# Optimization experiments

Measured on AMD Instinct MI355X. Metric: run time of the kernel, lower is better.

## Reference

```python
import jax, jax.numpy as jnp
import numpy as np

N, P, C, H, W = 2, 100, 256, 128, 192
K = 3; KK = K * K; E = C * KK; NH = 8; DH = E // NH; FFN = 2048


def _ln(x, g, b, eps=1e-5):
    m = x.mean(-1, keepdims=True)
    v = ((x - m) ** 2).mean(-1, keepdims=True)
    return (x - m) * jax.lax.rsqrt(v + eps) * g + b


def setup_inputs():
    ks = iter(jax.random.split(jax.random.key(0), 64))
    def rnd(shape, s=1.0):
        return jax.random.normal(next(ks), shape, jnp.float32) * s
    z = lambda *s: jnp.zeros(s, jnp.float32)
    o = lambda *s: jnp.ones(s, jnp.float32)
    return {
        'x': rnd((N, C, H, W)),
        'proposal_feat': rnd((N, P, E)),
        'mask_preds': rnd((N, P, H, W)),
        'ku_dyn_w': rnd((2 * C, C), 0.02), 'ku_dyn_b': z(2 * C),
        'ku_in_w': rnd((2 * C, C), 0.02), 'ku_in_b': z(2 * C),
        'ku_ig_w': rnd((C, C), 0.02), 'ku_ig_b': z(C),
        'ku_ug_w': rnd((C, C), 0.02), 'ku_ug_b': z(C),
        'ku_nin_g': o(C), 'ku_nin_b': z(C),
        'ku_nout_g': o(C), 'ku_nout_b': z(C),
        'ku_inin_g': o(C), 'ku_inin_b': z(C),
        'ku_inout_g': o(C), 'ku_inout_b': z(C),
        'ku_fc_w': rnd((C, C), 0.02), 'ku_fc_b': z(C),
        'ku_fcn_g': o(C), 'ku_fcn_b': z(C),
        'attn_in_w': rnd((3 * E, E), 0.02), 'attn_in_b': z(3 * E),
        'attn_out_w': rnd((E, E), 0.02), 'attn_out_b': z(E),
        'attn_ln_g': o(E), 'attn_ln_b': z(E),
        'ffn_w1': rnd((FFN, C), 0.02), 'ffn_b1': z(FFN),
        'ffn_w2': rnd((C, FFN), 0.02), 'ffn_b2': z(C),
        'ffn_ln_g': o(C), 'ffn_ln_b': z(C),
        'mask_fc_ws': rnd((3, C, C), 0.02),
        'mask_fc_ln_g': o(3, C), 'mask_fc_ln_b': z(3, C),
        'fc_mask_w': rnd((C, C), 0.02), 'fc_mask_b': z(C),
    }


def _forward(x, proposal_feat, mask_preds, ku_dyn_w, ku_dyn_b, ku_in_w, ku_in_b,
             ku_ig_w, ku_ig_b, ku_ug_w, ku_ug_b, ku_nin_g, ku_nin_b, ku_nout_g,
             ku_nout_b, ku_inin_g, ku_inin_b, ku_inout_g, ku_inout_b, ku_fc_w,
             ku_fc_b, ku_fcn_g, ku_fcn_b, attn_in_w, attn_in_b, attn_out_w,
             attn_out_b, attn_ln_g, attn_ln_b, ffn_w1, ffn_b1, ffn_w2, ffn_b2,
             ffn_ln_g, ffn_ln_b, mask_fc_ws, mask_fc_ln_g, mask_fc_ln_b,
             fc_mask_w, fc_mask_b):
    # mask-softmax pooling over proposals: (N,P,H,W) x (N,C,H,W) -> (N,P,C)
    sig = jax.nn.softmax(mask_preds, axis=1)
    x_feat = jnp.einsum('bnhw,bchw->bnc', sig, x)

    # KernelUpdator (gated dynamic kernel update)
    pf = proposal_feat.reshape(N, P, C, KK).transpose(0, 1, 3, 2).reshape(N * P, KK, C)
    upd = x_feat.reshape(N * P, C)
    params = upd @ ku_dyn_w.T + ku_dyn_b            # (NP, 2C)
    p_in, p_out = params[:, :C], params[:, C:]
    inp = pf @ ku_in_w.T + ku_in_b                  # (NP, KK, 2C)
    i_in, i_out = inp[..., :C], inp[..., C:]
    gate = i_in * p_in[:, None, :]                  # (NP, KK, C)
    ig = jax.nn.sigmoid(_ln(gate @ ku_ig_w.T + ku_ig_b, ku_inin_g, ku_inin_b))
    ug = jax.nn.sigmoid(_ln(gate @ ku_ug_w.T + ku_ug_b, ku_nin_g, ku_nin_b))
    p_out = _ln(p_out, ku_nout_g, ku_nout_b)
    i_out = _ln(i_out, ku_inout_g, ku_inout_b)
    feat = ug * p_out[:, None, :] + ig * i_out
    feat = jax.nn.relu(_ln(feat @ ku_fc_w.T + ku_fc_b, ku_fcn_g, ku_fcn_b))  # (NP,KK,C)

    # self-attention across proposals; embed dim E = C*K*K, with residual + LN
    obj = feat.reshape(N, P, E).transpose(1, 0, 2)  # (P,N,E)
    qkv = obj @ attn_in_w.T + attn_in_b
    q, k, v = jnp.split(qkv, 3, axis=-1)
    q = q.reshape(P, N, NH, DH) * np.float32(1.0 / np.sqrt(DH))
    k = k.reshape(P, N, NH, DH)
    v = v.reshape(P, N, NH, DH)
    a = jax.nn.softmax(jnp.einsum('qnhd,knhd->nhqk', q, k), axis=-1)
    o = jnp.einsum('nhqk,knhd->qnhd', a, v).reshape(P, N, E)
    obj = _ln(obj + o @ attn_out_w.T + attn_out_b, attn_ln_g, attn_ln_b)
    obj = obj.transpose(1, 0, 2).reshape(N, P, KK, C)

    # FFN (residual) + LN, applied per (proposal, kernel position)
    h = jax.nn.relu(obj @ ffn_w1.T + ffn_b1) @ ffn_w2.T + ffn_b2
    obj = _ln(obj + h, ffn_ln_g, ffn_ln_b)

    mf = obj
    for i in range(3):
        mf = jax.nn.relu(_ln(mf @ mask_fc_ws[i].T, mask_fc_ln_g[i], mask_fc_ln_b[i]))
    mf = mf @ fc_mask_w.T + fc_mask_b               # (N,P,KK,C)
    kernels = mf.transpose(0, 1, 3, 2).reshape(N, P, C, K, K)

    # per-image dynamic conv: vmap replaces the python loop over batch
    def conv_one(xi, wi):
        return jax.lax.conv_general_dilated(
            xi[None], wi, (1, 1), 'SAME',
            dimension_numbers=('NCHW', 'OIHW', 'NCHW'))[0]
    new_masks = jax.vmap(conv_one)(x, kernels)      # (N,P,H,W)

    obj_kernels = obj.transpose(0, 1, 3, 2).reshape(N, P, C, K, K)
    return new_masks, obj_kernels


def reference(x, proposal_feat, mask_preds, ku_dyn_w, ku_dyn_b, ku_in_w, ku_in_b,
              ku_ig_w, ku_ig_b, ku_ug_w, ku_ug_b, ku_nin_g, ku_nin_b, ku_nout_g,
              ku_nout_b, ku_inin_g, ku_inin_b, ku_inout_g, ku_inout_b, ku_fc_w,
              ku_fc_b, ku_fcn_g, ku_fcn_b, attn_in_w, attn_in_b, attn_out_w,
              attn_out_b, attn_ln_g, attn_ln_b, ffn_w1, ffn_b1, ffn_w2, ffn_b2,
              ffn_ln_g, ffn_ln_b, mask_fc_ws, mask_fc_ln_g, mask_fc_ln_b,
              fc_mask_w, fc_mask_b):
    return _forward(x, proposal_feat, mask_preds, ku_dyn_w, ku_dyn_b, ku_in_w,
                    ku_in_b, ku_ig_w, ku_ig_b, ku_ug_w, ku_ug_b, ku_nin_g,
                    ku_nin_b, ku_nout_g, ku_nout_b, ku_inin_g, ku_inin_b,
                    ku_inout_g, ku_inout_b, ku_fc_w, ku_fc_b, ku_fcn_g, ku_fcn_b,
                    attn_in_w, attn_in_b, attn_out_w, attn_out_b, attn_ln_g,
                    attn_ln_b, ffn_w1, ffn_b1, ffn_w2, ffn_b2, ffn_ln_g,
                    ffn_ln_b, mask_fc_ws, mask_fc_ln_g, mask_fc_ln_b,
                    fc_mask_w, fc_mask_b)
```

## Files before the change

kernel.cpp:

```cpp
#include <hip/hip_runtime.h>
#include <hip/hip_bf16.h>

#define N_ 2
#define P_ 100
#define C_ 256
#define H_ 128
#define W_ 192
#define HW_ 24576
#define KK_ 9
#define E_ 2304
#define NH_ 8
#define DH_ 288
#define FFN_ 2048
#define NP_ 200
#define ROWS_ 1800
#define XKC_ 64

typedef __attribute__((ext_vector_type(8))) __bf16 bf16x8;
typedef __attribute__((ext_vector_type(4))) float f32x4;

__global__ __launch_bounds__(256) void k_softmax(const float* __restrict__ mp, float* __restrict__ sig){
  int idx = blockIdx.x*256 + threadIdx.x;
  if(idx >= N_*HW_) return;
  int n = idx / HW_, hw = idx - n*HW_;
  const float* base = mp + (size_t)n*P_*HW_ + hw;
  float m = -1e30f;
  for(int p=0;p<P_;p++) m = fmaxf(m, base[(size_t)p*HW_]);
  float s = 0.f;
  for(int p=0;p<P_;p++) s += __expf(base[(size_t)p*HW_] - m);
  float inv = 1.f/s;
  float* ob = sig + (size_t)n*P_*HW_ + hw;
  for(int p=0;p<P_;p++) ob[(size_t)p*HW_] = __expf(base[(size_t)p*HW_] - m)*inv;
}

__global__ __launch_bounds__(256) void k_permute_pf(const float* __restrict__ prop, float* __restrict__ pf){
  int i = blockIdx.x*256 + threadIdx.x;
  if(i >= ROWS_*C_) return;
  int c = i & 255;
  int r = i >> 8;
  int kk = r % 9, np = r / 9;
  pf[i] = prop[(size_t)np*E_ + c*KK_ + kk];
}

__global__ __launch_bounds__(256) void k_xfeat1m(const float* __restrict__ sig, const float* __restrict__ x,
                                                 float* __restrict__ partial){
  const int ct = blockIdx.x, kb = blockIdx.y, n = blockIdx.z;
  const int hw0 = kb*384;
  const int tid = threadIdx.x;
  const int wid = tid >> 6, lane = tid & 63;
  const int col = lane & 15, quad = lane >> 4;
  const int wm = wid & 1, wn = wid >> 1;
  const int MT = wm ? 3 : 4;
  __shared__ __bf16 As[112][72];
  __shared__ __bf16 Bs[128][72];
  f32x4 acc[4][4] = {};
  for(int k0=0; k0<384; k0+=64){
    __syncthreads();
    for(int i=tid; i<896; i+=256){
      int p = i >> 3, kg = i & 7;
      bf16x8 v;
      if(p < P_){
        const float* sp = &sig[((size_t)n*P_ + p)*HW_ + hw0 + k0 + kg*8];
        const float4 f0 = *(const float4*)sp;
        const float4 f1 = *(const float4*)(sp+4);
        v[0]=(__bf16)f0.x; v[1]=(__bf16)f0.y; v[2]=(__bf16)f0.z; v[3]=(__bf16)f0.w;
        v[4]=(__bf16)f1.x; v[5]=(__bf16)f1.y; v[6]=(__bf16)f1.z; v[7]=(__bf16)f1.w;
      } else {
        #pragma unroll
        for(int u=0;u<8;u++) v[u] = (__bf16)0.f;
      }
      *(bf16x8*)&As[p][kg*8] = v;
    }
    for(int i=tid; i<1024; i+=256){
      int c = i >> 3, kg = i & 7;
      const float* xp = &x[((size_t)n*C_ + ct*128 + c)*HW_ + hw0 + k0 + kg*8];
      const float4 f0 = *(const float4*)xp;
      const float4 f1 = *(const float4*)(xp+4);
      bf16x8 v;
      v[0]=(__bf16)f0.x; v[1]=(__bf16)f0.y; v[2]=(__bf16)f0.z; v[3]=(__bf16)f0.w;
      v[4]=(__bf16)f1.x; v[5]=(__bf16)f1.y; v[6]=(__bf16)f1.z; v[7]=(__bf16)f1.w;
      *(bf16x8*)&Bs[c][kg*8] = v;
    }
    __syncthreads();
    #pragma unroll
    for(int ks=0; ks<2; ks++){
      bf16x8 b[4];
      #pragma unroll
      for(int t=0;t<4;t++) b[t] = *(const bf16x8*)&Bs[(wn*4+t)*16 + col][ks*32 + quad*8];
      #pragma unroll
      for(int mt=0; mt<4; mt++){
        if(mt < MT){
          bf16x8 a = *(const bf16x8*)&As[(wm*4+mt)*16 + col][ks*32 + quad*8];
          #pragma unroll
          for(int t=0;t<4;t++)
            acc[mt][t] = __builtin_amdgcn_mfma_f32_16x16x32_bf16(a, b[t], acc[mt][t], 0, 0, 0);
        }
      }
    }
  }
  #pragma unroll
  for(int mt=0; mt<4; mt++){
    if(mt < MT){
      #pragma unroll
      for(int r=0;r<4;r++){
        int p = (wm*4+mt)*16 + quad*4 + r;
        if(p < P_){
          float* op = &partial[(((size_t)n*XKC_ + kb)*P_ + p)*C_ + ct*128 + wn*64 + col];
          #pragma unroll
          for(int t=0;t<4;t++) op[t*16] = acc[mt][t][r];
        }
      }
    }
  }
}

__global__ __launch_bounds__(256) void k_xfeat2(const float* __restrict__ partial, float* __restrict__ xfeat){
  int np = blockIdx.x;
  int n = np / P_, p = np - n*P_;
  int c = threadIdx.x;
  float s = 0.f;
  for(int kb=0;kb<XKC_;kb++) s += partial[(((size_t)n*XKC_ + kb)*P_ + p)*C_ + c];
  xfeat[(size_t)np*C_ + c] = s;
}

__global__ __launch_bounds__(256) void k_gemm_mfma(const float* __restrict__ A, const float* __restrict__ Wt,
    const float* __restrict__ bias, float* __restrict__ out, int M, int N, int K, int act)
{
  const int n0 = blockIdx.x*128, m0 = blockIdx.y*64;
  const int tid = threadIdx.x;
  const int wid = tid >> 6, lane = tid & 63;
  const int col = lane & 15, quad = lane >> 4;
  const int wm = wid & 1, wn = wid >> 1;
  __shared__ __bf16 As[64][72];
  __shared__ __bf16 Bs[128][72];
  f32x4 acc[2][4] = {};
  for(int k0=0; k0<K; k0+=64){
    __syncthreads();
    for(int i=tid; i<512; i+=256){
      int r = i >> 3, kg = i & 7;
      int m = m0 + r;
      bf16x8 v;
      if(m < M){
        const float* ap = &A[(size_t)m*K + k0 + kg*8];
        const float4 f0 = *(const float4*)ap;
        const float4 f1 = *(const float4*)(ap+4);
        v[0]=(__bf16)f0.x; v[1]=(__bf16)f0.y; v[2]=(__bf16)f0.z; v[3]=(__bf16)f0.w;
        v[4]=(__bf16)f1.x; v[5]=(__bf16)f1.y; v[6]=(__bf16)f1.z; v[7]=(__bf16)f1.w;
      } else {
        #pragma unroll
        for(int u=0;u<8;u++) v[u] = (__bf16)0.f;
      }
      *(bf16x8*)&As[r][kg*8] = v;
    }
    for(int i=tid; i<1024; i+=256){
      int r = i >> 3, kg = i & 7;
      const float* wp = &Wt[(size_t)(n0 + r)*K + k0 + kg*8];
      const float4 f0 = *(const float4*)wp;
      const float4 f1 = *(const float4*)(wp+4);
      bf16x8 v;
      v[0]=(__bf16)f0.x; v[1]=(__bf16)f0.y; v[2]=(__bf16)f0.z; v[3]=(__bf16)f0.w;
      v[4]=(__bf16)f1.x; v[5]=(__bf16)f1.y; v[6]=(__bf16)f1.z; v[7]=(__bf16)f1.w;
      *(bf16x8*)&Bs[r][kg*8] = v;
    }
    __syncthreads();
    #pragma unroll
    for(int ks=0; ks<2; ks++){
      bf16x8 b[4], a[2];
      #pragma unroll
      for(int t=0;t<4;t++) b[t] = *(const bf16x8*)&Bs[(wn*4+t)*16 + col][ks*32 + quad*8];
      #pragma unroll
      for(int mt=0;mt<2;mt++) a[mt] = *(const bf16x8*)&As[(wm*2+mt)*16 + col][ks*32 + quad*8];
      #pragma unroll
      for(int mt=0;mt<2;mt++)
        #pragma unroll
        for(int t=0;t<4;t++)
          acc[mt][t] = __builtin_amdgcn_mfma_f32_16x16x32_bf16(a[mt], b[t], acc[mt][t], 0, 0, 0);
    }
  }
  #pragma unroll
  for(int mt=0;mt<2;mt++){
    #pragma unroll
    for(int r=0;r<4;r++){
      int m = m0 + (wm*2+mt)*16 + quad*4 + r;
      if(m < M){
        #pragma unroll
        for(int t=0;t<4;t++){
          int n = n0 + (wn*4+t)*16 + col;
          float v = acc[mt][t][r];
          if(bias) v += bias[n];
          if(act == 1) v = fmaxf(v, 0.f);
          if(act == 3) ((__bf16*)out)[(size_t)m*N + n] = (__bf16)v;
          else out[(size_t)m*N + n] = v;
        }
      }
    }
  }
}

__global__ __launch_bounds__(256) void k_gemm_skM256(const float* __restrict__ A, const float* __restrict__ Wt,
    float* __restrict__ part, int M, int N, int K, int KC)
{
  const int n0 = blockIdx.x*64;
  const int kz = blockIdx.y*KC;
  const int tid = threadIdx.x;
  const int wid = tid >> 6, lane = tid & 63;
  const int col = lane & 15, quad = lane >> 4;
  const int wm = wid & 1, wn = wid >> 1;
  __shared__ __bf16 As[256][72];
  __shared__ __bf16 Bs[64][72];
  f32x4 acc[8][2] = {};
  for(int k0=kz; k0<kz+KC; k0+=64){
    __syncthreads();
    for(int i=tid; i<2048; i+=256){
      int r = i >> 3, kg = i & 7;
      bf16x8 v;
      if(r < M){
        const float* ap = &A[(size_t)r*K + k0 + kg*8];
        const float4 f0 = *(const float4*)ap;
        const float4 f1 = *(const float4*)(ap+4);
        v[0]=(__bf16)f0.x; v[1]=(__bf16)f0.y; v[2]=(__bf16)f0.z; v[3]=(__bf16)f0.w;
        v[4]=(__bf16)f1.x; v[5]=(__bf16)f1.y; v[6]=(__bf16)f1.z; v[7]=(__bf16)f1.w;
      } else {
        #pragma unroll
        for(int u=0;u<8;u++) v[u] = (__bf16)0.f;
      }
      *(bf16x8*)&As[r][kg*8] = v;
    }
    for(int i=tid; i<512; i+=256){
      int r = i >> 3, kg = i & 7;
      const float* wp = &Wt[(size_t)(n0 + r)*K + k0 + kg*8];
      const float4 f0 = *(const float4*)wp;
      const float4 f1 = *(const float4*)(wp+4);
      bf16x8 v;
      v[0]=(__bf16)f0.x; v[1]=(__bf16)f0.y; v[2]=(__bf16)f0.z; v[3]=(__bf16)f0.w;
      v[4]=(__bf16)f1.x; v[5]=(__bf16)f1.y; v[6]=(__bf16)f1.z; v[7]=(__bf16)f1.w;
      *(bf16x8*)&Bs[r][kg*8] = v;
    }
    __syncthreads();
    #pragma unroll
    for(int ks=0; ks<2; ks++){
      bf16x8 b[2];
      #pragma unroll
      for(int t=0;t<2;t++) b[t] = *(const bf16x8*)&Bs[(wn*2+t)*16 + col][ks*32 + quad*8];
      #pragma unroll
      for(int mt=0;mt<8;mt++){
        bf16x8 a = *(const bf16x8*)&As[(wm*8+mt)*16 + col][ks*32 + quad*8];
        #pragma unroll
        for(int t=0;t<2;t++)
          acc[mt][t] = __builtin_amdgcn_mfma_f32_16x16x32_bf16(a, b[t], acc[mt][t], 0, 0, 0);
      }
    }
  }
  float* pbase = part + (size_t)blockIdx.y*M*N;
  #pragma unroll
  for(int mt=0;mt<8;mt++){
    #pragma unroll
    for(int r=0;r<4;r++){
      int m = (wm*8+mt)*16 + quad*4 + r;
      if(m < M){
        #pragma unroll
        for(int t=0;t<2;t++){
          int n = n0 + (wn*2+t)*16 + col;
          pbase[(size_t)m*N + n] = acc[mt][t][r];
        }
      }
    }
  }
}

__global__ __launch_bounds__(256) void k_gemm_splitk(const float* __restrict__ A, const float* __restrict__ Wt,
    float* __restrict__ part, int M, int N, int K, int KC, int PX, int MY)
{
  const int wg = blockIdx.x;
  const int xcd = wg & 7, slot = wg >> 3;
  const int mb = slot % MY, pg = slot / MY;
  const int panel = xcd + 8*pg;
  const int PZ = K / KC;
  if(panel >= PX*PZ) return;
  const int px = panel % PX, pz = panel / PX;
  const int n0 = px*128, m0 = mb*64;
  const int kz = pz*KC;
  const int tid = threadIdx.x;
  const int wid = tid >> 6, lane = tid & 63;
  const int col = lane & 15, quad = lane >> 4;
  const int wm = wid & 1, wn = wid >> 1;
  __shared__ __bf16 As[64][72];
  __shared__ __bf16 Bs[128][72];
  f32x4 acc[2][4] = {};
  for(int k0=kz; k0<kz+KC; k0+=64){
    __syncthreads();
    for(int i=tid; i<512; i+=256){
      int r = i >> 3, kg = i & 7;
      int m = m0 + r;
      bf16x8 v;
      if(m < M){
        const float* ap = &A[(size_t)m*K + k0 + kg*8];
        const float4 f0 = *(const float4*)ap;
        const float4 f1 = *(const float4*)(ap+4);
        v[0]=(__bf16)f0.x; v[1]=(__bf16)f0.y; v[2]=(__bf16)f0.z; v[3]=(__bf16)f0.w;
        v[4]=(__bf16)f1.x; v[5]=(__bf16)f1.y; v[6]=(__bf16)f1.z; v[7]=(__bf16)f1.w;
      } else {
        #pragma unroll
        for(int u=0;u<8;u++) v[u] = (__bf16)0.f;
      }
      *(bf16x8*)&As[r][kg*8] = v;
    }
    for(int i=tid; i<1024; i+=256){
      int r = i >> 3, kg = i & 7;
      const float* wp = &Wt[(size_t)(n0 + r)*K + k0 + kg*8];
      const float4 f0 = *(const float4*)wp;
      const float4 f1 = *(const float4*)(wp+4);
      bf16x8 v;
      v[0]=(__bf16)f0.x; v[1]=(__bf16)f0.y; v[2]=(__bf16)f0.z; v[3]=(__bf16)f0.w;
      v[4]=(__bf16)f1.x; v[5]=(__bf16)f1.y; v[6]=(__bf16)f1.z; v[7]=(__bf16)f1.w;
      *(bf16x8*)&Bs[r][kg*8] = v;
    }
    __syncthreads();
    #pragma unroll
    for(int ks=0; ks<2; ks++){
      bf16x8 b[4], a[2];
      #pragma unroll
      for(int t=0;t<4;t++) b[t] = *(const bf16x8*)&Bs[(wn*4+t)*16 + col][ks*32 + quad*8];
      #pragma unroll
      for(int mt=0;mt<2;mt++) a[mt] = *(const bf16x8*)&As[(wm*2+mt)*16 + col][ks*32 + quad*8];
      #pragma unroll
      for(int mt=0;mt<2;mt++)
        #pragma unroll
        for(int t=0;t<4;t++)
          acc[mt][t] = __builtin_amdgcn_mfma_f32_16x16x32_bf16(a[mt], b[t], acc[mt][t], 0, 0, 0);
    }
  }
  float* pbase = part + (size_t)pz*M*N;
  #pragma unroll
  for(int mt=0;mt<2;mt++){
    #pragma unroll
    for(int r=0;r<4;r++){
      int m = m0 + (wm*2+mt)*16 + quad*4 + r;
      if(m < M){
        #pragma unroll
        for(int t=0;t<4;t++){
          int n = n0 + (wn*4+t)*16 + col;
          pbase[(size_t)m*N + n] = acc[mt][t][r];
        }
      }
    }
  }
}

__global__ __launch_bounds__(256) void k_redk(const float* __restrict__ part, const float* __restrict__ bias,
    float* __restrict__ out, int M, int N, int S)
{
  size_t i4 = ((size_t)blockIdx.x*256 + threadIdx.x)*4;
  size_t MN = (size_t)M*N;
  if(i4 >= MN) return;
  float4 s = *(const float4*)&part[i4];
  for(int z=1; z<S; z++){
    const float4 p = *(const float4*)&part[(size_t)z*MN + i4];
    s.x+=p.x; s.y+=p.y; s.z+=p.z; s.w+=p.w;
  }
  if(bias){
    int n = (int)(i4 % (size_t)N);
    const float4 b = *(const float4*)&bias[n];
    s.x+=b.x; s.y+=b.y; s.z+=b.z; s.w+=b.w;
  }
  *(float4*)&out[i4] = s;
}

__global__ __launch_bounds__(256) void k_ln256(const float* __restrict__ in, const float* __restrict__ res,
    const float* __restrict__ g, const float* __restrict__ b, float* __restrict__ out, int M, int act)
{
  int row = blockIdx.x*4 + (threadIdx.x >> 6);
  int lane = threadIdx.x & 63;
  if(row >= M) return;
  float4 v = *(const float4*)&in[(size_t)row*C_ + lane*4];
  if(res){
    const float4 rv = *(const float4*)&res[(size_t)row*C_ + lane*4];
    v.x += rv.x; v.y += rv.y; v.z += rv.z; v.w += rv.w;
  }
  float s = v.x + v.y + v.z + v.w;
  float q = v.x*v.x + v.y*v.y + v.z*v.z + v.w*v.w;
  #pragma unroll
  for(int off=32; off; off>>=1){ s += __shfl_xor(s, off, 64); q += __shfl_xor(q, off, 64); }
  float mean = s*(1.f/256.f);
  float rstd = rsqrtf(q*(1.f/256.f) - mean*mean + 1e-5f);
  const float4 gv = *(const float4*)&g[lane*4];
  const float4 bv = *(const float4*)&b[lane*4];
  float o[4] = {(v.x-mean)*rstd*gv.x + bv.x, (v.y-mean)*rstd*gv.y + bv.y,
                (v.z-mean)*rstd*gv.z + bv.z, (v.w-mean)*rstd*gv.w + bv.w};
  #pragma unroll
  for(int j=0;j<4;j++){
    if(act==1) o[j] = fmaxf(o[j], 0.f);
    else if(act==2) o[j] = 1.f/(1.f + __expf(-o[j]));
  }
  float4 ov = {o[0],o[1],o[2],o[3]};
  *(float4*)&out[(size_t)row*C_ + lane*4] = ov;
}

__global__ __launch_bounds__(256) void k_gate(const float* __restrict__ inp, const float* __restrict__ params,
                                              float* __restrict__ gate){
  int i = blockIdx.x*256 + threadIdx.x;
  if(i >= ROWS_*C_) return;
  int c = i & 255, r = i >> 8;
  int np = r / 9;
  gate[i] = inp[(size_t)r*512 + c] * params[(size_t)np*512 + c];
}

__device__ __forceinline__ void block_stats(float v, float* red, int slot, float& mean, float& rstd){
  float s = v, q = v*v;
  #pragma unroll
  for(int off=32; off; off>>=1){ s += __shfl_xor(s, off, 64); q += __shfl_xor(q, off, 64); }
  int wid = threadIdx.x >> 6;
  if((threadIdx.x & 63) == 0){ red[slot + wid] = s; red[slot + 4 + wid] = q; }
  __syncthreads();
  s = red[slot+0]+red[slot+1]+red[slot+2]+red[slot+3];
  q = red[slot+4]+red[slot+5]+red[slot+6]+red[slot+7];
  mean = s*(1.f/256.f);
  rstd = rsqrtf(q*(1.f/256.f) - mean*mean + 1e-5f);
}

__global__ __launch_bounds__(256) void k_combine(const float* __restrict__ params, const float* __restrict__ inp,
  const float* __restrict__ ug, const float* __restrict__ ig,
  const float* __restrict__ nout_g, const float* __restrict__ nout_b,
  const float* __restrict__ inout_g, const float* __restrict__ inout_b,
  float* __restrict__ feat)
{
  __shared__ float red[16];
  int r = blockIdx.x;
  int np = r / 9;
  int c = threadIdx.x;
  float pv = params[(size_t)np*512 + 256 + c];
  float mean, rstd;
  block_stats(pv, red, 0, mean, rstd);
  float pn = (pv - mean)*rstd*nout_g[c] + nout_b[c];
  float iv = inp[(size_t)r*512 + 256 + c];
  float mean2, rstd2;
  block_stats(iv, red, 8, mean2, rstd2);
  float iw = (iv - mean2)*rstd2*inout_g[c] + inout_b[c];
  size_t o = (size_t)r*C_ + c;
  feat[o] = ug[o]*pn + ig[o]*iw;
}

__global__ __launch_bounds__(256) void k_attn2(const float* __restrict__ qkv, float* __restrict__ attnO){
  const int qt = blockIdx.x, h = blockIdx.y, n = blockIdx.z;
  const int q0 = qt*10;
  const int tid = threadIdx.x;
  __shared__ float Qs[10][292];
  __shared__ float KVs[25][292];
  __shared__ float Ss[10][104];
  const float scale = 0.05892556509887896f;
  const size_t base = (size_t)n*P_*6912 + (size_t)h*DH_;
  for(int i=tid; i<10*DH_; i+=256){
    int qi = i/DH_, d = i - qi*DH_;
    Qs[qi][d] = qkv[base + (size_t)(q0+qi)*6912 + d] * scale;
  }
  for(int kt=0; kt<4; kt++){
    int kp0 = kt*25;
    __syncthreads();
    for(int i=tid; i<25*DH_; i+=256){
      int ki = i/DH_, d = i - ki*DH_;
      KVs[ki][d] = qkv[base + (size_t)(kp0+ki)*6912 + E_ + d];
    }
    __syncthreads();
    if(tid < 250){
      int qi = tid/25, ki = tid - qi*25;
      float s = 0.f;
      #pragma unroll 9
      for(int d=0; d<DH_; d+=4){
        const float4 a = *(const float4*)&Qs[qi][d];
        const float4 b = *(const float4*)&KVs[ki][d];
        s += a.x*b.x + a.y*b.y + a.z*b.z + a.w*b.w;
      }
      Ss[qi][kp0+ki] = s;
    }
  }
  __syncthreads();
  {
    int w = tid >> 6, lane = tid & 63;
    for(int r=w; r<10; r+=4){
      float v0 = (lane < 100) ? Ss[r][lane] : -1e30f;
      float v1 = (lane < 36)  ? Ss[r][64+lane] : -1e30f;
      float m = fmaxf(v0, v1);
      #pragma unroll
      for(int off=32; off; off>>=1) m = fmaxf(m, __shfl_xor(m, off, 64));
      float e0 = (lane < 100) ? __expf(v0-m) : 0.f;
      float e1 = (lane < 36)  ? __expf(v1-m) : 0.f;
      float s = e0 + e1;
      #pragma unroll
      for(int off=32; off; off>>=1) s += __shfl_xor(s, off, 64);
      float inv = 1.f/s;
      if(lane < 100) Ss[r][lane] = e0*inv;
      if(lane < 36)  Ss[r][64+lane] = e1*inv;
    }
  }
  float acc[12];
  #pragma unroll
  for(int j=0;j<12;j++) acc[j]=0.f;
  for(int kt=0; kt<4; kt++){
    int kp0 = kt*25;
    __syncthreads();
    for(int i=tid; i<25*DH_; i+=256){
      int ki = i/DH_, d = i - ki*DH_;
      KVs[ki][d] = qkv[base + (size_t)(kp0+ki)*6912 + 2*E_ + d];
    }
    __syncthreads();
    int j = 0;
    for(int i=tid; i<10*DH_; i+=256, j++){
      int qi = i/DH_, d = i - qi*DH_;
      float s = acc[j];
      #pragma unroll
      for(int ki=0; ki<25; ki++) s += Ss[qi][kp0+ki]*KVs[ki][d];
      acc[j] = s;
    }
  }
  {
    int j = 0;
    for(int i=tid; i<10*DH_; i+=256, j++){
      int qi = i/DH_, d = i - qi*DH_;
      attnO[(size_t)(n*P_ + q0 + qi)*E_ + h*DH_ + d] = acc[j];
    }
  }
}

__global__ __launch_bounds__(256) void k_add_ln2304(const float* __restrict__ obj0, const float* __restrict__ tp,
  const float* __restrict__ g, const float* __restrict__ b, float* __restrict__ out)
{
  __shared__ float red[8];
  int row = blockIdx.x;
  float v[9]; float s=0.f, q=0.f;
  #pragma unroll
  for(int j=0;j<9;j++){
    int e = threadIdx.x + j*256;
    float t = obj0[(size_t)row*E_ + e] + tp[(size_t)row*E_ + e];
    v[j]=t; s+=t; q+=t*t;
  }
  #pragma unroll
  for(int off=32; off; off>>=1){ s += __shfl_xor(s, off, 64); q += __shfl_xor(q, off, 64); }
  int wid = threadIdx.x>>6;
  if((threadIdx.x&63)==0){ red[wid]=s; red[4+wid]=q; }
  __syncthreads();
  s = red[0]+red[1]+red[2]+red[3]; q = red[4]+red[5]+red[6]+red[7];
  float mean = s*(1.f/2304.f);
  float rstd = rsqrtf(q*(1.f/2304.f) - mean*mean + 1e-5f);
  #pragma unroll
  for(int j=0;j<9;j++){
    int e = threadIdx.x + j*256;
    out[(size_t)row*E_ + e] = (v[j]-mean)*rstd*g[e] + b[e];
  }
}

__global__ __launch_bounds__(256) void k_objk(const float* __restrict__ obj2, float* __restrict__ outk){
  int i = blockIdx.x*256 + threadIdx.x;
  if(i >= ROWS_*C_) return;
  int kk = i % 9; int t = i / 9; int c = t & 255; int np = t >> 8;
  outk[i] = obj2[((size_t)np*9 + kk)*C_ + c];
}

__global__ __launch_bounds__(256) void k_prep_x(const float* __restrict__ x, __bf16* __restrict__ xT){
  int i = blockIdx.x*256 + threadIdx.x;
  if(i >= N_*32*H_*W_) return;
  int w = i % W_; int t = i / W_;
  int h = t % H_; t /= H_;
  int g = t % 32; int n = t / 32;
  const float* xp = &x[((size_t)(n*C_ + g*8)*H_ + h)*W_ + w];
  bf16x8 v;
  #pragma unroll
  for(int u=0;u<8;u++) v[u] = (__bf16)xp[(size_t)u*HW_];
  *(bf16x8*)&xT[(size_t)i*8] = v;
}

__global__ __launch_bounds__(256) void k_permute_ker(const __bf16* __restrict__ mfFb, __bf16* __restrict__ kerP){
  int i = blockIdx.x*256 + threadIdx.x;
  if(i >= 73728) return;
  int pl = i & 63; int t = i >> 6;
  int oct = t & 3; t >>= 2;
  int tap = t % 9; t /= 9;
  int c0b = t & 7; int nps = t >> 3;
  int n = nps >> 1, ps = nps & 1;
  int p = ps*64 + pl;
  bf16x8 v;
  if(p < P_){
    v = *(const bf16x8*)&mfFb[((size_t)(n*P_+p)*9 + tap)*C_ + c0b*32 + oct*8];
  } else {
    #pragma unroll
    for(int u=0;u<8;u++) v[u] = (__bf16)0.f;
  }
  *(bf16x8*)&kerP[(size_t)i*8] = v;
}

__global__ __launch_bounds__(256) void k_conv_mfma(const __bf16* __restrict__ xT, const __bf16* __restrict__ kerP,
                                                   float* __restrict__ out){
  const int wt = blockIdx.x, ht = blockIdx.y, z = blockIdx.z;
  const int n = z >> 1, ps = z & 1;
  const int pbase = ps*64;
  const int NT = ps ? 3 : 4;
  const int tid = threadIdx.x;
  const int hi = tid >> 6;
  const int lane = tid & 63;
  const int col = lane & 15, quad = lane >> 4;
  const int w0 = wt*64, h0 = ht*4;

  __shared__ __bf16 xs[6][4][66][8];
  __shared__ __bf16 ks[9][4][64][8];
  __bf16* ksf = &ks[0][0][0][0];

  f32x4 acc[4][4] = {};

  for(int c0=0; c0<C_; c0+=32){
    __syncthreads();
    for(int i=tid; i<1584; i+=256){
      int oct = i / 396;
      int rem = i - oct*396;
      int hy = rem / 66, wx = rem - hy*66;
      int hh = h0 - 1 + hy, ww = w0 - 1 + wx;
      bf16x8 v;
      if(hh >= 0 && hh < H_ && ww >= 0 && ww < W_){
        v = *(const bf16x8*)&xT[((((size_t)n*32 + (c0>>3) + oct)*H_ + hh)*W_ + ww)*8];
      } else {
        #pragma unroll
        for(int u=0;u<8;u++) v[u] = (__bf16)0.f;
      }
      *(bf16x8*)&xs[hy][oct][wx][0] = v;
    }
    {
      const __bf16* kp = kerP + ((size_t)(n*2+ps)*8 + (c0>>5))*2304*8;
      for(int i=tid; i<2304; i+=256)
        *(bf16x8*)&ksf[(size_t)i*8] = *(const bf16x8*)&kp[(size_t)i*8];
    }
    __syncthreads();
    #pragma unroll
    for(int ky=0; ky<3; ky++){
      #pragma unroll
      for(int kx=0; kx<3; kx++){
        const int tap = ky*3 + kx;
        const int hy = hi + ky;
        bf16x8 b[4];
        #pragma unroll
        for(int t=0;t<4;t++) b[t] = *(const bf16x8*)&xs[hy][quad][t*16 + col + kx][0];
        #pragma unroll
        for(int pt=0; pt<4; pt++){
          if(pt < NT){
            bf16x8 a = *(const bf16x8*)&ks[tap][quad][pt*16 + col][0];
            #pragma unroll
            for(int t=0;t<4;t++)
              acc[pt][t] = __builtin_amdgcn_mfma_f32_16x16x32_bf16(a, b[t], acc[pt][t], 0, 0, 0);
          }
        }
      }
    }
  }
  const int h = h0 + hi;
  #pragma unroll
  for(int pt=0; pt<4; pt++){
    if(pt < NT){
      #pragma unroll
      for(int r=0;r<4;r++){
        int p = pbase + pt*16 + quad*4 + r;
        if(p < P_){
          float* op = &out[((size_t)(n*P_+p)*H_ + h)*W_ + w0 + col];
          #pragma unroll
          for(int t=0;t<4;t++) op[t*16] = acc[pt][t][r];
        }
      }
    }
  }
}

extern "C" void kernel_launch(void* const* d_in, const int* in_sizes, int n_in,
                              void* d_out, int out_size, void* d_ws, size_t ws_size,
                              hipStream_t stream)
{
  (void)in_sizes; (void)n_in; (void)out_size; (void)ws_size;
  const float* x          = (const float*)d_in[0];
  const float* prop       = (const float*)d_in[1];
  const float* mask_pred  = (const float*)d_in[2];
  const float* ku_dyn_w   = (const float*)d_in[3];
  const float* ku_dyn_b   = (const float*)d_in[4];
  const float* ku_in_w    = (const float*)d_in[5];
  const float* ku_in_b    = (const float*)d_in[6];
  const float* ku_ig_w    = (const float*)d_in[7];
  const float* ku_ig_b    = (const float*)d_in[8];
  const float* ku_ug_w    = (const float*)d_in[9];
  const float* ku_ug_b    = (const float*)d_in[10];
  const float* ku_nin_g   = (const float*)d_in[11];
  const float* ku_nin_b   = (const float*)d_in[12];
  const float* ku_nout_g  = (const float*)d_in[13];
  const float* ku_nout_b  = (const float*)d_in[14];
  const float* ku_inin_g  = (const float*)d_in[15];
  const float* ku_inin_b  = (const float*)d_in[16];
  const float* ku_inout_g = (const float*)d_in[17];
  const float* ku_inout_b = (const float*)d_in[18];
  const float* ku_fc_w    = (const float*)d_in[19];
  const float* ku_fc_b    = (const float*)d_in[20];
  const float* ku_fcn_g   = (const float*)d_in[21];
  const float* ku_fcn_b   = (const float*)d_in[22];
  const float* attn_in_w  = (const float*)d_in[23];
  const float* attn_in_b  = (const float*)d_in[24];
  const float* attn_out_w = (const float*)d_in[25];
  const float* attn_out_b = (const float*)d_in[26];
  const float* attn_ln_g  = (const float*)d_in[27];
  const float* attn_ln_b  = (const float*)d_in[28];
  const float* ffn_w1     = (const float*)d_in[29];
  const float* ffn_b1     = (const float*)d_in[30];
  const float* ffn_w2     = (const float*)d_in[31];
  const float* ffn_b2     = (const float*)d_in[32];
  const float* ffn_ln_g   = (const float*)d_in[33];
  const float* ffn_ln_b   = (const float*)d_in[34];
  const float* mask_fc_ws = (const float*)d_in[35];
  const float* mask_fc_ln_g = (const float*)d_in[36];
  const float* mask_fc_ln_b = (const float*)d_in[37];
  const float* fc_mask_w  = (const float*)d_in[38];
  const float* fc_mask_b  = (const float*)d_in[39];

  float* ws = (float*)d_ws;
  float* sig     = ws;
  float* hbuf    = ws;
  float* skA     = ws;
  float* partial = ws + 4915200;
  float* skB     = ws + 4915200;
  float* attnO   = ws + 4915200 + 1382400;
  float* tproj   = ws + 4915200 + 1843200;
  float* tmp     = ws + 4915200 + 2304000;
  float* qkv     = ws + 8294400;
  float* xfeat   = ws + 9830400;
  float* params  = xfeat + 51200;
  float* pf      = params + 102400;
  float* inp     = pf + 460800;
  float* gate    = inp + 921600;
  float* ig      = gate + 460800;
  float* ug      = ig + 460800;
  float* feat    = ug + 460800;
  float* obj0    = feat + 460800;
  float* obj1    = obj0 + 460800;
  float* obj2    = obj1 + 460800;
  float* mf1     = obj2 + 460800;
  float* mf2     = mf1 + 460800;
  float* mfF     = mf2 + 460800;
  __bf16* xT = (__bf16*)ws;
  __bf16* kerP = (__bf16*)(ws + 6758400);

  float* out_masks = (float*)d_out;
  float* out_kern  = out_masks + (size_t)N_*P_*HW_;

  k_softmax<<<192, 256, 0, stream>>>(mask_pred, sig);
  k_permute_pf<<<1800, 256, 0, stream>>>(prop, pf);
  k_xfeat1m<<<dim3(2,XKC_,2), 256, 0, stream>>>(sig, x, partial);
  k_xfeat2<<<200, 256, 0, stream>>>(partial, xfeat);
  k_gemm_mfma<<<dim3(4,4),   256, 0, stream>>>(xfeat, ku_dyn_w, ku_dyn_b, params, 200, 512, 256, 0);
  k_gemm_mfma<<<dim3(4,29),  256, 0, stream>>>(pf, ku_in_w, ku_in_b, inp, 1800, 512, 256, 0);
  k_gate<<<1800, 256, 0, stream>>>(inp, params, gate);
  k_gemm_mfma<<<dim3(2,29),  256, 0, stream>>>(gate, ku_ig_w, ku_ig_b, tmp, 1800, 256, 256, 0);
  k_ln256<<<450, 256, 0, stream>>>(tmp, nullptr, ku_inin_g, ku_inin_b, ig, 1800, 2);
  k_gemm_mfma<<<dim3(2,29),  256, 0, stream>>>(gate, ku_ug_w, ku_ug_b, tmp, 1800, 256, 256, 0);
  k_ln256<<<450, 256, 0, stream>>>(tmp, nullptr, ku_nin_g, ku_nin_b, ug, 1800, 2);
  k_combine<<<1800, 256, 0, stream>>>(params, inp, ug, ig, ku_nout_g, ku_nout_b, ku_inout_g, ku_inout_b, feat);
  k_gemm_mfma<<<dim3(2,29),  256, 0, stream>>>(feat, ku_fc_w, ku_fc_b, tmp, 1800, 256, 256, 0);
  k_ln256<<<450, 256, 0, stream>>>(tmp, nullptr, ku_fcn_g, ku_fcn_b, obj0, 1800, 1);
  k_gemm_skM256<<<dim3(108,6), 256, 0, stream>>>(obj0, attn_in_w, skA, 200, 6912, 2304, 384);
  k_redk<<<1350, 256, 0, stream>>>(skA, attn_in_b, qkv, 200, 6912, 6);
  k_attn2<<<dim3(10,8,2), 256, 0, stream>>>(qkv, attnO);
  k_gemm_skM256<<<dim3(36,9), 256, 0, stream>>>(attnO, attn_out_w, skA, 200, 2304, 2304, 256);
  k_redk<<<450, 256, 0, stream>>>(skA, attn_out_b, tproj, 200, 2304, 9);
  k_add_ln2304<<<200, 256, 0, stream>>>(obj0, tproj, attn_ln_g, attn_ln_b, obj1);
  k_gemm_mfma<<<dim3(16,29), 256, 0, stream>>>(obj1, ffn_w1, ffn_b1, hbuf, 1800, 2048, 256, 1);
  k_gemm_splitk<<<232, 256, 0, stream>>>(hbuf, ffn_w2, skB, 1800, 256, 2048, 512, 2, 29);
  k_redk<<<450, 256, 0, stream>>>(skB, ffn_b2, tmp, 1800, 256, 4);
  k_ln256<<<450, 256, 0, stream>>>(tmp, obj1, ffn_ln_g, ffn_ln_b, obj2, 1800, 0);
  k_gemm_mfma<<<dim3(2,29),  256, 0, stream>>>(obj2, mask_fc_ws,          nullptr, tmp, 1800, 256, 256, 0);
  k_ln256<<<450, 256, 0, stream>>>(tmp, nullptr, mask_fc_ln_g,       mask_fc_ln_b,       mf1, 1800, 1);
  k_gemm_mfma<<<dim3(2,29),  256, 0, stream>>>(mf1,  mask_fc_ws + 65536,  nullptr, tmp, 1800, 256, 256, 0);
  k_ln256<<<450, 256, 0, stream>>>(tmp, nullptr, mask_fc_ln_g + 256, mask_fc_ln_b + 256, mf2, 1800, 1);
  k_gemm_mfma<<<dim3(2,29),  256, 0, stream>>>(mf2,  mask_fc_ws + 131072, nullptr, tmp, 1800, 256, 256, 0);
  k_ln256<<<450, 256, 0, stream>>>(tmp, nullptr, mask_fc_ln_g + 512, mask_fc_ln_b + 512, mf1, 1800, 1);
  k_gemm_mfma<<<dim3(2,29),  256, 0, stream>>>(mf1, fc_mask_w, fc_mask_b, mfF, 1800, 256, 256, 3);
  k_objk<<<1800, 256, 0, stream>>>(obj2, out_kern);
  k_permute_ker<<<288, 256, 0, stream>>>((const __bf16*)mfF, kerP);
  k_prep_x<<<6144, 256, 0, stream>>>(x, xT);
  k_conv_mfma<<<dim3(3,32,4), 256, 0, stream>>>(xT, kerP, out_masks);
}
```

Measured before the change: 722.4 us.

## Prefetch next channel chunk into registers while computing current conv chunk

Restructures the conv MFMA kernel's channel loop into a register-staged software pipeline. The global loads for the next 32-channel chunk of input and kernel go into registers before the MFMA work of the current chunk, so their latency overlaps with compute. Address and bounds computation is hoisted out of the loop into precomputed offsets and LDS pointers. In exchange it uses many more vector registers (16 bf16x8 staging values plus pointers), which may reduce occupancy or cause spills.

After: 717.0 us. No clear change (-0.7%).

```diff
diff --git a/kernel.cpp b/kernel.cpp
--- a/kernel.cpp
+++ b/kernel.cpp
@@ -605,28 +605,49 @@
 
   f32x4 acc[4][4] = {};
 
-  for(int c0=0; c0<C_; c0+=32){
-    __syncthreads();
-    for(int i=tid; i<1584; i+=256){
-      int oct = i / 396;
-      int rem = i - oct*396;
-      int hy = rem / 66, wx = rem - hy*66;
+  int xoff[7];
+  __bf16* xlds[7];
+  #pragma unroll
+  for(int j=0;j<7;j++){
+    int i = tid + j*256;
+    if(i < 1584){
+      int oct = i/396; int rem = i - oct*396;
+      int hy = rem/66, wx = rem - hy*66;
       int hh = h0 - 1 + hy, ww = w0 - 1 + wx;
-      bf16x8 v;
-      if(hh >= 0 && hh < H_ && ww >= 0 && ww < W_){
-        v = *(const bf16x8*)&xT[((((size_t)n*32 + (c0>>3) + oct)*H_ + hh)*W_ + ww)*8];
-      } else {
-        #pragma unroll
-        for(int u=0;u<8;u++) v[u] = (__bf16)0.f;
-      }
-      *(bf16x8*)&xs[hy][oct][wx][0] = v;
-    }
-    {
-      const __bf16* kp = kerP + ((size_t)(n*2+ps)*8 + (c0>>5))*2304*8;
-      for(int i=tid; i<2304; i+=256)
-        *(bf16x8*)&ksf[(size_t)i*8] = *(const bf16x8*)&kp[(size_t)i*8];
-    }
-    __syncthreads();
+      xlds[j] = &xs[hy][oct][wx][0];
+      xoff[j] = (hh>=0 && hh<H_ && ww>=0 && ww<W_) ? (((n*32+oct)*H_ + hh)*W_ + ww)*8 : -1;
+    } else { xlds[j] = nullptr; xoff[j] = -1; }
+  }
+  const __bf16* kbase = kerP + (size_t)(n*2+ps)*8*2304*8;
+
+  bf16x8 xv[7], kv[9];
+  bf16x8 zro;
+  #pragma unroll
+  for(int u=0;u<8;u++) zro[u] = (__bf16)0.f;
+  #pragma unroll
+  for(int j=0;j<7;j++) xv[j] = zro;
+  #pragma unroll
+  for(int j=0;j<7;j++)
+    if(xoff[j] >= 0) xv[j] = *(const bf16x8*)&xT[xoff[j]];
+  #pragma unroll
+  for(int j=0;j<9;j++) kv[j] = *(const bf16x8*)&kbase[(size_t)(tid + j*256)*8];
+
+  for(int s=0; s<8; s++){
+    __syncthreads();
+    #pragma unroll
+    for(int j=0;j<7;j++)
+      if(tid + j*256 < 1584) *(bf16x8*)xlds[j] = xv[j];
+    #pragma unroll
+    for(int j=0;j<9;j++) *(bf16x8*)&ksf[(size_t)(tid + j*256)*8] = kv[j];
+    __syncthreads();
+    if(s < 7){
+      #pragma unroll
+      for(int j=0;j<7;j++)
+        if(xoff[j] >= 0) xv[j] = *(const bf16x8*)&xT[xoff[j] + (s+1)*786432];
+      const __bf16* kb2 = kbase + (size_t)(s+1)*18432;
+      #pragma unroll
+      for(int j=0;j<9;j++) kv[j] = *(const bf16x8*)&kb2[(size_t)(tid + j*256)*8];
+    }
     #pragma unroll
     for(int ky=0; ky<3; ky++){
       #pragma unroll
```
